# Kernel optimization log

Measured on AMD Instinct MI355X. Metric: run time of the kernel, lower is better.

## Reference

```python
import jax, jax.numpy as jnp
import numpy as np

NEG = -1e30  # finite stand-in for -inf (keeps grads nan-free)
BLANK = 0


def _ctc_nll(log_probs, targets, input_lengths, target_lengths):
    """Per-sample CTC negative log-likelihood.
    log_probs: (B,T,V) log-softmax outputs; targets: (B,S) int; lengths: (B,)."""
    B, T, V = log_probs.shape
    S = targets.shape[1]
    L = 2 * S + 1
    # extended label sequence: blank, y1, blank, y2, ..., blank -> (B, L)
    ext = jnp.full((B, L), BLANK, dtype=targets.dtype).at[:, 1::2].set(targets)
    # skip transition (l-2 -> l) allowed iff ext[l] != blank and ext[l] != ext[l-2]
    prev2 = jnp.pad(ext[:, :-2], ((0, 0), (2, 0)), constant_values=-1)
    skip = (ext != BLANK) & (ext != prev2)  # (B, L)

    def emit(lp_t):  # lp_t: (B,V) -> (B,L)
        return jnp.take_along_axis(lp_t, ext, axis=1)

    alpha0 = jnp.where(jnp.arange(L)[None, :] < 2, emit(log_probs[:, 0]), NEG)

    def step(alpha, lp_t):
        p1 = jnp.pad(alpha[:, :-1], ((0, 0), (1, 0)), constant_values=NEG)
        p2 = jnp.pad(alpha[:, :-2], ((0, 0), (2, 0)), constant_values=NEG)
        p2 = jnp.where(skip, p2, NEG)
        m = jnp.maximum(alpha, jnp.maximum(p1, p2))
        lse = m + jnp.log(jnp.exp(alpha - m) + jnp.exp(p1 - m) + jnp.exp(p2 - m))
        new = lse + emit(lp_t)
        return new, new

    # scan over time; collect alphas so we can read them at each sample's T_b-1
    _, alphas_rest = jax.lax.scan(step, alpha0, jnp.swapaxes(log_probs, 0, 1)[1:])
    alphas = jnp.concatenate([alpha0[None], alphas_rest], axis=0)  # (T,B,L)
    alphas = jnp.swapaxes(alphas, 0, 1)  # (B,T,L)
    alpha_T = jnp.take_along_axis(
        alphas, (input_lengths - 1)[:, None, None], axis=1)[:, 0]  # (B,L)

    end1 = jnp.take_along_axis(alpha_T, (2 * target_lengths)[:, None], axis=1)[:, 0]
    end2 = jnp.take_along_axis(alpha_T, (2 * target_lengths - 1)[:, None], axis=1)[:, 0]
    m = jnp.maximum(end1, end2)
    ll = m + jnp.log(jnp.exp(end1 - m) + jnp.exp(end2 - m))
    return -ll  # (B,)


def setup_inputs() -> dict:
    key = jax.random.key(0)
    k1, k2, k3, k4 = jax.random.split(key, 4)
    B, T, V, S = 32, 2000, 1024, 256
    log_probs = jax.nn.log_softmax(
        jax.random.normal(k1, (B, T, V), dtype=jnp.float32), axis=-1)
    targets = jax.random.randint(k2, (B, S), 1, V)  # exclude blank=0
    input_lengths = jax.random.randint(k3, (B,), 1500, T + 1)
    target_lengths = jax.random.randint(k4, (B,), 128, S + 1)
    return {"log_probs": log_probs, "targets": targets,
            "input_lengths": input_lengths, "target_lengths": target_lengths}


def reference(log_probs, targets, input_lengths, target_lengths):
    nll = _ctc_nll(log_probs, targets, input_lengths, target_lengths)
    # zero_infinity=True: drop infeasible samples
    nll = jnp.where(nll > 0.5 * (-NEG), 0.0, nll)
    # reduction='mean': divide each loss by its target length, then batch-mean
    return jnp.mean(nll / target_lengths.astype(nll.dtype))
```

## Files before the change

### kernel.cpp

```cpp
#include <hip/hip_runtime.h>
#include <stdint.h>


#define CS 32
#define TT 8
#define LN2F 0.69314718055994530942f

#define ASYNC_CP16(g, l)                                                     \
  __builtin_amdgcn_global_load_lds(                                          \
      (__attribute__((address_space(1))) void*)(g),                          \
      (__attribute__((address_space(3))) void*)(l), 16, 0, 0)
#define ASYNC_CP4(g, l)                                                      \
  __builtin_amdgcn_global_load_lds(                                          \
      (__attribute__((address_space(1))) void*)(g),                          \
      (__attribute__((address_space(3))) void*)(l), 4, 0, 0)

__device__ __forceinline__ float shr1f(float x) {
  return __int_as_float(
      __builtin_amdgcn_update_dpp(0, __float_as_int(x), 0x138, 0xF, 0xF, true));
}
__device__ __forceinline__ int shr1i(int x) {
  return __builtin_amdgcn_update_dpp(0, x, 0x138, 0xF, 0xF, true);
}

__global__ __launch_bounds__(256) void k_gather_exp(
    const float* __restrict__ lp, const int* __restrict__ tgt,
    const int* __restrict__ ilen, float* __restrict__ El,
    float* __restrict__ Eb, int T, int V, int S) {
  const int b = blockIdx.y;
  const int t0 = blockIdx.x * TT;
  const int tid = threadIdx.x;
  __shared__ int labs[256];
  labs[tid] = tgt[b * S + tid];
  const int Tb = ilen[b];
  __syncthreads();
  const int rn = min(TT, Tb - t0);
  if (rn <= 0) return;
  const int lab = labs[tid];
  const float* rowp = lp + ((size_t)b * T + t0) * V;
  float* outp = El + ((size_t)b * T + t0) * S + tid;
  if (rn == TT) {
    float v[TT];
#pragma unroll
    for (int r = 0; r < TT; ++r) v[r] = rowp[(size_t)r * V + lab];
#pragma unroll
    for (int r = 0; r < TT; ++r) outp[(size_t)r * S] = __expf(v[r]);
  } else {
    for (int r = 0; r < rn; ++r) outp[(size_t)r * S] = __expf(rowp[(size_t)r * V + lab]);
  }
  if (tid < rn) Eb[(size_t)b * T + t0 + tid] = __expf(rowp[(size_t)tid * V]);
}

__global__ __launch_bounds__(64) void k_ctc_alpha(
    const float* __restrict__ El, const float* __restrict__ Eb,
    const int* __restrict__ tgt, const int* __restrict__ ilen,
    const int* __restrict__ tlen, float* __restrict__ nll_out, int T, int S) {
  const int b = blockIdx.x;
  const int lane = threadIdx.x;
  const bool l0 = (lane == 0);
  __shared__ __align__(16) float elbuf[2][CS][256];
  __shared__ float ebbuf[2][CS];

  const int Tb = ilen[b];
  const int U = tlen[b];

  const int4 tg = *(const int4*)(tgt + (size_t)b * S + 4 * lane);
  const int tprev = __shfl_up(tg.w, 1);
  const float sk0 = (l0 || tg.x != tprev) ? 1.0f : 0.0f;
  const float sk1 = (tg.y != tg.x) ? 1.0f : 0.0f;
  const float sk2 = (tg.z != tg.y) ? 1.0f : 0.0f;
  const float sk3 = (tg.w != tg.z) ? 1.0f : 0.0f;

  float aL0 = 0, aL1 = 0, aL2 = 0, aL3 = 0;
  float aB0 = 0, aB1 = 0, aB2 = 0, aB3 = 0;
  float a0 = 0;
  int o = 0;
  float s = 1.0f;

  const float* Elb = El + (size_t)b * T * 256;
  const float* Ebb = Eb + (size_t)b * T;

  {
    const int nrows = min(CS, T);
    for (int r = 0; r < nrows; ++r)
      ASYNC_CP16(Elb + (size_t)r * 256 + 4 * lane, &elbuf[0][r][0]);
    if (lane < nrows) ASYNC_CP4(Ebb + lane, &ebbuf[0][0]);
  }

  auto stepf = [&](float4 el, float eb) {
    float pL = shr1f(aL3) * s;
    float pB = shr1f(aB3) * s;
    pL = l0 ? 0.0f : pL;
    pB = l0 ? a0 : pB;
    const float nB0 = (aB0 + aL0) * eb;
    const float nB1 = (aB1 + aL1) * eb;
    const float nB2 = (aB2 + aL2) * eb;
    const float nB3 = (aB3 + aL3) * eb;
    const float nL0 = (aL0 + pB + sk0 * pL) * el.x;
    const float nL1 = (aL1 + aB0 + sk1 * aL0) * el.y;
    const float nL2 = (aL2 + aB1 + sk2 * aL1) * el.z;
    const float nL3 = (aL3 + aB2 + sk3 * aL2) * el.w;
    a0 *= eb;
    aL0 = nL0; aL1 = nL1; aL2 = nL2; aL3 = nL3;
    aB0 = nB0; aB1 = nB1; aB2 = nB2; aB3 = nB3;
  };
  auto renorm = [&]() {
    float m = fmaxf(fmaxf(fmaxf(aL0, aL1), fmaxf(aL2, aL3)),
                    fmaxf(fmaxf(aB0, aB1), fmaxf(aB2, aB3)));
    m = fmaxf(m, a0);
    const bool nz = (m > 0.0f);
    const int mk = nz ? (((__float_as_int(m) >> 23) & 0xff) - 126) : 0;
    const int ocand = o + mk;
    const int oleft = shr1i(ocand);
    o = (nz || l0) ? ocand : oleft;
    const float sc = nz ? __int_as_float((127 - mk) << 23) : 1.0f;
    aL0 *= sc; aL1 *= sc; aL2 *= sc; aL3 *= sc;
    aB0 *= sc; aB1 *= sc; aB2 *= sc; aB3 *= sc;
    a0 *= sc;
    int d = shr1i(o) - o;
    d = max(-126, min(126, d));
    s = __int_as_float((d + 127) << 23);
  };

  const int nchunks = (Tb + CS - 1) / CS;
  for (int c = 0; c < nchunks; ++c) {
    asm volatile("s_waitcnt vmcnt(0)" ::: "memory");
    __syncthreads();
    const int buf = c & 1;
    if ((c + 1) * CS < Tb) {
      const int base = (c + 1) * CS;
      const int nrows = min(CS, T - base);
      const float* gEl = Elb + (size_t)base * 256 + 4 * lane;
      for (int r = 0; r < nrows; ++r)
        ASYNC_CP16(gEl + (size_t)r * 256, &elbuf[buf ^ 1][r][0]);
      if (lane < nrows) ASYNC_CP4(Ebb + base + lane, &ebbuf[buf ^ 1][0]);
    }
    const int nsteps = min(CS, Tb - c * CS);

    float4 ce[4]; float cb[4];
#pragma unroll
    for (int j = 0; j < 4; ++j) {
      ce[j] = *(const float4*)&elbuf[buf][j][4 * lane];
      cb[j] = ebbuf[buf][j];
    }
    for (int g = 0; g < nsteps; g += 4) {
      float4 ne[4]; float nb[4];
      const bool pf = (g + 4 < CS);
      if (pf) {
#pragma unroll
        for (int j = 0; j < 4; ++j) {
          ne[j] = *(const float4*)&elbuf[buf][g + 4 + j][4 * lane];
          nb[j] = ebbuf[buf][g + 4 + j];
        }
      }
      if (g + 4 <= nsteps) {
        if (c == 0 && g == 0) {
          a0 = l0 ? cb[0] : 0.0f;
          aL0 = l0 ? ce[0].x : 0.0f;
          aL1 = aL2 = aL3 = aB0 = aB1 = aB2 = aB3 = 0.0f;
          stepf(ce[1], cb[1]); stepf(ce[2], cb[2]); stepf(ce[3], cb[3]);
        } else {
          stepf(ce[0], cb[0]); stepf(ce[1], cb[1]);
          stepf(ce[2], cb[2]); stepf(ce[3], cb[3]);
        }
        renorm();
      } else {
#pragma unroll
        for (int j = 0; j < 4; ++j) {
          if (g + j < nsteps) {
            if (c == 0 && g == 0 && j == 0) {
              a0 = l0 ? cb[0] : 0.0f;
              aL0 = l0 ? ce[0].x : 0.0f;
              aL1 = aL2 = aL3 = aB0 = aB1 = aB2 = aB3 = 0.0f;
            } else {
              stepf(ce[j], cb[j]);
            }
          }
        }
      }
      if (pf) {
#pragma unroll
        for (int j = 0; j < 4; ++j) { ce[j] = ne[j]; cb[j] = nb[j]; }
      }
    }
  }

  if (lane == ((U - 1) >> 2)) {
    const int j = (U - 1) & 3;
    float sv;
    if (j == 0)      sv = aL0 + aB0;
    else if (j == 1) sv = aL1 + aB1;
    else if (j == 2) sv = aL2 + aB2;
    else             sv = aL3 + aB3;
    float nll = -LN2F * (__log2f(sv) + (float)o);
    if (!(nll < 5e29f)) nll = 0.0f;
    nll_out[b] = nll / (float)U;
  }
}

__global__ __launch_bounds__(64) void k_reduce(const float* __restrict__ nll,
                                               float* __restrict__ out,
                                               int B) {
  float v = 0.0f;
  for (int i = threadIdx.x; i < B; i += 64) v += nll[i];
  for (int off = 32; off > 0; off >>= 1) v += __shfl_down(v, off);
  if (threadIdx.x == 0) out[0] = v / (float)B;
}

extern "C" void kernel_launch(void* const* d_in, const int* in_sizes, int n_in,
                              void* d_out, int out_size, void* d_ws,
                              size_t ws_size, hipStream_t stream) {
  const float* lp = (const float*)d_in[0];
  const int* tgt = (const int*)d_in[1];
  const int* ilen = (const int*)d_in[2];
  const int* tlen = (const int*)d_in[3];

  const int B = in_sizes[2];
  const int S = in_sizes[1] / B;
  const int V = 1024;
  const int T = (int)((size_t)in_sizes[0] / ((size_t)B * V));

  float* El = (float*)d_ws;
  float* Eb = El + (size_t)B * T * S;
  float* nw = Eb + (size_t)B * T;

  dim3 g1((T + TT - 1) / TT, B);
  k_gather_exp<<<g1, 256, 0, stream>>>(lp, tgt, ilen, El, Eb, T, V, S);
  k_ctc_alpha<<<B, 64, 0, stream>>>(El, Eb, tgt, ilen, tlen, nw, T, S);
  k_reduce<<<1, 64, 0, stream>>>(nw, (float*)d_out, B);
}
```

Before: 579.6 us.

## Replace LDS double-buffered alpha staging with register prefetch ring; one-row gather blocks

After: 512.9 us. 11.5% less time.

```diff
diff --git a/kernel.cpp b/kernel.cpp
--- a/kernel.cpp
+++ b/kernel.cpp
@@ -2,18 +2,8 @@
 #include <stdint.h>
 
 
-#define CS 32
-#define TT 8
 #define LN2F 0.69314718055994530942f
-
-#define ASYNC_CP16(g, l)                                                     \
-  __builtin_amdgcn_global_load_lds(                                          \
-      (__attribute__((address_space(1))) void*)(g),                          \
-      (__attribute__((address_space(3))) void*)(l), 16, 0, 0)
-#define ASYNC_CP4(g, l)                                                      \
-  __builtin_amdgcn_global_load_lds(                                          \
-      (__attribute__((address_space(1))) void*)(g),                          \
-      (__attribute__((address_space(3))) void*)(l), 4, 0, 0)
+#define PD 16
 
 __device__ __forceinline__ float shr1f(float x) {
   return __int_as_float(
@@ -28,27 +18,13 @@
     const int* __restrict__ ilen, float* __restrict__ El,
     float* __restrict__ Eb, int T, int V, int S) {
   const int b = blockIdx.y;
-  const int t0 = blockIdx.x * TT;
+  const int t = blockIdx.x;
+  if (t >= ilen[b]) return;
   const int tid = threadIdx.x;
-  __shared__ int labs[256];
-  labs[tid] = tgt[b * S + tid];
-  const int Tb = ilen[b];
-  __syncthreads();
-  const int rn = min(TT, Tb - t0);
-  if (rn <= 0) return;
-  const int lab = labs[tid];
-  const float* rowp = lp + ((size_t)b * T + t0) * V;
-  float* outp = El + ((size_t)b * T + t0) * S + tid;
-  if (rn == TT) {
-    float v[TT];
-#pragma unroll
-    for (int r = 0; r < TT; ++r) v[r] = rowp[(size_t)r * V + lab];
-#pragma unroll
-    for (int r = 0; r < TT; ++r) outp[(size_t)r * S] = __expf(v[r]);
-  } else {
-    for (int r = 0; r < rn; ++r) outp[(size_t)r * S] = __expf(rowp[(size_t)r * V + lab]);
-  }
-  if (tid < rn) Eb[(size_t)b * T + t0 + tid] = __expf(rowp[(size_t)tid * V]);
+  const int lab = tgt[b * S + tid];
+  const float* row = lp + ((size_t)b * T + t) * V;
+  El[((size_t)b * T + t) * S + tid] = __expf(row[lab]);
+  if (tid == 0) Eb[(size_t)b * T + t] = __expf(row[0]);
 }
 
 __global__ __launch_bounds__(64) void k_ctc_alpha(
@@ -58,8 +34,6 @@
   const int b = blockIdx.x;
   const int lane = threadIdx.x;
   const bool l0 = (lane == 0);
-  __shared__ __align__(16) float elbuf[2][CS][256];
-  __shared__ float ebbuf[2][CS];
 
   const int Tb = ilen[b];
   const int U = tlen[b];
@@ -71,21 +45,15 @@
   const float sk2 = (tg.z != tg.y) ? 1.0f : 0.0f;
   const float sk3 = (tg.w != tg.z) ? 1.0f : 0.0f;
 
-  float aL0 = 0, aL1 = 0, aL2 = 0, aL3 = 0;
-  float aB0 = 0, aB1 = 0, aB2 = 0, aB3 = 0;
-  float a0 = 0;
-  int o = 0;
-  float s = 1.0f;
-
   const float* Elb = El + (size_t)b * T * 256;
   const float* Ebb = Eb + (size_t)b * T;
 
-  {
-    const int nrows = min(CS, T);
-    for (int r = 0; r < nrows; ++r)
-      ASYNC_CP16(Elb + (size_t)r * 256 + 4 * lane, &elbuf[0][r][0]);
-    if (lane < nrows) ASYNC_CP4(Ebb + lane, &ebbuf[0][0]);
-  }
+  float a0 = l0 ? Ebb[0] : 0.0f;
+  float aL0 = l0 ? Elb[0] : 0.0f;
+  float aL1 = 0, aL2 = 0, aL3 = 0;
+  float aB0 = 0, aB1 = 0, aB2 = 0, aB3 = 0;
+  int o = 0;
+  float s = 1.0f;
 
   auto stepf = [&](float4 el, float eb) {
     float pL = shr1f(aL3) * s;
@@ -96,10 +64,10 @@
     const float nB1 = (aB1 + aL1) * eb;
     const float nB2 = (aB2 + aL2) * eb;
     const float nB3 = (aB3 + aL3) * eb;
-    const float nL0 = (aL0 + pB + sk0 * pL) * el.x;
-    const float nL1 = (aL1 + aB0 + sk1 * aL0) * el.y;
-    const float nL2 = (aL2 + aB1 + sk2 * aL1) * el.z;
-    const float nL3 = (aL3 + aB2 + sk3 * aL2) * el.w;
+    const float nL0 = (aL0 + fmaf(sk0, pL, pB)) * el.x;
+    const float nL1 = (aL1 + fmaf(sk1, aL0, aB0)) * el.y;
+    const float nL2 = (aL2 + fmaf(sk2, aL1, aB1)) * el.z;
+    const float nL3 = (aL3 + fmaf(sk3, aL2, aB2)) * el.w;
     a0 *= eb;
     aL0 = nL0; aL1 = nL1; aL2 = nL2; aL3 = nL3;
     aB0 = nB0; aB1 = nB1; aB2 = nB2; aB3 = nB3;
@@ -122,65 +90,40 @@
     s = __int_as_float((d + 127) << 23);
   };
 
-  const int nchunks = (Tb + CS - 1) / CS;
-  for (int c = 0; c < nchunks; ++c) {
-    asm volatile("s_waitcnt vmcnt(0)" ::: "memory");
-    __syncthreads();
-    const int buf = c & 1;
-    if ((c + 1) * CS < Tb) {
-      const int base = (c + 1) * CS;
-      const int nrows = min(CS, T - base);
-      const float* gEl = Elb + (size_t)base * 256 + 4 * lane;
-      for (int r = 0; r < nrows; ++r)
-        ASYNC_CP16(gEl + (size_t)r * 256, &elbuf[buf ^ 1][r][0]);
-      if (lane < nrows) ASYNC_CP4(Ebb + base + lane, &ebbuf[buf ^ 1][0]);
+  float4 pel[PD];
+  float peb[PD];
+  const int lo4 = 4 * lane;
+
+#pragma unroll
+  for (int j = 0; j < PD; ++j) {
+    const int row = min(j + 1, Tb - 1);
+    pel[j] = *(const float4*)(Elb + ((size_t)row << 8) + lo4);
+    peb[j] = Ebb[row];
+  }
+
+  const int R = Tb - 1;
+  const int nfull = R >> 4;
+  const int rem = R & 15;
+
+  for (int k = 0; k < nfull; ++k) {
+    const int base = 1 + (k << 4);
+#pragma unroll
+    for (int j = 0; j < PD; ++j) {
+      const float4 el = pel[j];
+      const float eb = peb[j];
+      const int row = min(base + PD + j, Tb - 1);
+      pel[j] = *(const float4*)(Elb + ((size_t)row << 8) + lo4);
+      peb[j] = Ebb[row];
+      stepf(el, eb);
+      if ((j & 3) == 2) renorm();
     }
-    const int nsteps = min(CS, Tb - c * CS);
-
-    float4 ce[4]; float cb[4];
+  }
+  {
 #pragma unroll
-    for (int j = 0; j < 4; ++j) {
-      ce[j] = *(const float4*)&elbuf[buf][j][4 * lane];
-      cb[j] = ebbuf[buf][j];
-    }
-    for (int g = 0; g < nsteps; g += 4) {
-      float4 ne[4]; float nb[4];
-      const bool pf = (g + 4 < CS);
-      if (pf) {
-#pragma unroll
-        for (int j = 0; j < 4; ++j) {
-          ne[j] = *(const float4*)&elbuf[buf][g + 4 + j][4 * lane];
-          nb[j] = ebbuf[buf][g + 4 + j];
-        }
-      }
-      if (g + 4 <= nsteps) {
-        if (c == 0 && g == 0) {
-          a0 = l0 ? cb[0] : 0.0f;
-          aL0 = l0 ? ce[0].x : 0.0f;
-          aL1 = aL2 = aL3 = aB0 = aB1 = aB2 = aB3 = 0.0f;
-          stepf(ce[1], cb[1]); stepf(ce[2], cb[2]); stepf(ce[3], cb[3]);
-        } else {
-          stepf(ce[0], cb[0]); stepf(ce[1], cb[1]);
-          stepf(ce[2], cb[2]); stepf(ce[3], cb[3]);
-        }
-        renorm();
-      } else {
-#pragma unroll
-        for (int j = 0; j < 4; ++j) {
-          if (g + j < nsteps) {
-            if (c == 0 && g == 0 && j == 0) {
-              a0 = l0 ? cb[0] : 0.0f;
-              aL0 = l0 ? ce[0].x : 0.0f;
-              aL1 = aL2 = aL3 = aB0 = aB1 = aB2 = aB3 = 0.0f;
-            } else {
-              stepf(ce[j], cb[j]);
-            }
-          }
-        }
-      }
-      if (pf) {
-#pragma unroll
-        for (int j = 0; j < 4; ++j) { ce[j] = ne[j]; cb[j] = nb[j]; }
+    for (int j = 0; j < PD; ++j) {
+      if (j < rem) {
+        stepf(pel[j], peb[j]);
+        if ((j & 3) == 2) renorm();
       }
     }
   }
@@ -224,7 +167,7 @@
   float* Eb = El + (size_t)B * T * S;
   float* nw = Eb + (size_t)B * T;
 
-  dim3 g1((T + TT - 1) / TT, B);
+  dim3 g1(T, B);
   k_gather_exp<<<g1, 256, 0, stream>>>(lp, tgt, ilen, El, Eb, T, V, S);
   k_ctc_alpha<<<B, 64, 0, stream>>>(El, Eb, tgt, ilen, tlen, nw, T, S);
   k_reduce<<<1, 64, 0, stream>>>(nw, (float*)d_out, B);
```
